# Kernel tuning notes

Hardware: AMD Instinct MI355X
Metric: run time of the kernel (lower is better)

## Reference

```python
import jax, jax.numpy as jnp
import numpy as np

N, C, S = 2, 512, 256
SCALE = 2.0

def setup_inputs() -> dict:
    key = jax.random.key(0)
    kq, kk, kv = jax.random.split(key, 3)
    q = jax.random.normal(kq, (N, C, S), dtype=jnp.float32)
    k = jax.random.normal(kk, (N, C, S), dtype=jnp.float32)
    v = jax.random.normal(kv, (N, C, S), dtype=jnp.float32)
    return {"q": q, "k": k, "v": v}

def reference(q, k, v):
    # q: (N,C,S) -> (N,C,1,S); k: (N,C,S) -> (N,1,C,S)
    # weights[n,c,d] = -sum_s |k[n,d,s] - q[n,c,s]| / scale
    diff = jnp.abs(k[:, None, :, :] - q[:, :, None, :])  # (N,C,C,S)
    weights = -(diff / SCALE).sum(axis=-1)               # (N,C,C)
    weights = jax.nn.softmax(weights, axis=-1)
    rep = jnp.einsum('ncd,nds->ncs', weights, v)         # (N,C,S)
    return rep
```

## Files before the change

### kernel.cpp

```cpp
#include <hip/hip_runtime.h>


constexpr int N_  = 2;
constexpr int C_  = 512;
constexpr int S_  = 256;
constexpr int TC  = 4;
constexpr int NT  = 512;
constexpr int NW  = NT / 64;
constexpr int SC  = 32;
constexpr int SCQ = SC / 4;
constexpr int NCH = S_ / SC;
constexpr int KF  = C_ * SCQ / NT;

template <int CTRL, int ROW_MASK>
__device__ __forceinline__ float dpp_add(float x) {
    int yi = __builtin_amdgcn_update_dpp(0, __float_as_int(x), CTRL, ROW_MASK, 0xf, true);
    return x + __int_as_float(yi);
}
template <int CTRL, int ROW_MASK>
__device__ __forceinline__ float dpp_max(float x) {
    int yi = __builtin_amdgcn_update_dpp(__float_as_int(x), __float_as_int(x), CTRL, ROW_MASK, 0xf, false);
    return fmaxf(x, __int_as_float(yi));
}
__device__ __forceinline__ float wave_sum_bcast(float x) {
    x = dpp_add<0x111, 0xf>(x);
    x = dpp_add<0x112, 0xf>(x);
    x = dpp_add<0x114, 0xf>(x);
    x = dpp_add<0x118, 0xf>(x);
    x = dpp_add<0x142, 0xa>(x);
    x = dpp_add<0x143, 0xc>(x);
    return __int_as_float(__builtin_amdgcn_readlane(__float_as_int(x), 63));
}
__device__ __forceinline__ float wave_max_bcast(float x) {
    x = dpp_max<0x111, 0xf>(x);
    x = dpp_max<0x112, 0xf>(x);
    x = dpp_max<0x114, 0xf>(x);
    x = dpp_max<0x118, 0xf>(x);
    x = dpp_max<0x142, 0xa>(x);
    x = dpp_max<0x143, 0xc>(x);
    return __int_as_float(__builtin_amdgcn_readlane(__float_as_int(x), 63));
}
__device__ __forceinline__ void fma4(float4& a, const float s, const float4& v) {
    a.x += s * v.x; a.y += s * v.y; a.z += s * v.z; a.w += s * v.w;
}

__global__ __launch_bounds__(NT, 1)
void laplace_attn_fused(const float* __restrict__ qg,
                        const float* __restrict__ kg,
                        const float* __restrict__ vg,
                        float* __restrict__ out) {
    __shared__ __align__(16) float ksm[2][C_][SC];
    __shared__ __align__(16) float qs[TC][S_];
    __shared__ __align__(16) float wt[C_][TC];
    __shared__ float4 red1[NW];
    __shared__ float4 red2[NW];
    float4 (*po)[TC][S_ / 4] = (float4 (*)[TC][S_ / 4])&ksm[0][0][0];

    const int b    = blockIdx.x;
    const int n    = b & 1;
    const int c0   = (b >> 1) * TC;
    const int tid  = threadIdx.x;
    const int w    = tid >> 6;
    const int lane = tid & 63;

    const float* kn = kg + (size_t)n * C_ * S_;
    const float* vn = vg + (size_t)n * C_ * S_;
    const float* qn = qg + ((size_t)n * C_ + c0) * S_;

    if (tid < TC * (S_ / 4)) {
        const int row = tid >> 6;
        const int col = (tid & 63) << 2;
        *(float4*)&qs[row][col] = *(const float4*)(qn + (size_t)row * S_ + col);
    }

    const int srow = tid >> 3;
    const int sqo  = tid & 7;
    const int sp   = (sqo + srow) & 7;

    float4 greg[KF];
    #pragma unroll
    for (int it = 0; it < KF; ++it) {
        const int row = srow + (it << 6);
        greg[it] = *(const float4*)(kn + (size_t)row * S_ + (sqo << 2));
    }
    #pragma unroll
    for (int it = 0; it < KF; ++it) {
        const int row = srow + (it << 6);
        *(float4*)&ksm[0][row][sp << 2] = greg[it];
    }
    __syncthreads();

    float dist0 = 0.f, dist1 = 0.f, dist2 = 0.f, dist3 = 0.f;
    int cur = 0;

    for (int ch = 0; ch < NCH; ++ch) {
        if (ch + 1 < NCH) {
            const float* kc = kn + (ch + 1) * SC;
            #pragma unroll
            for (int it = 0; it < KF; ++it) {
                const int row = srow + (it << 6);
                greg[it] = *(const float4*)(kc + (size_t)row * S_ + (sqo << 2));
            }
        }
        const int sb = ch * SC;
        #pragma unroll
        for (int j = 0; j < SCQ; ++j) {
            const int p = (j + tid) & 7;
            const float4 kf = *(const float4*)&ksm[cur][tid][p << 2];
            const int s = sb + (j << 2);
            const float4 qa = *(const float4*)&qs[0][s];
            const float4 qb = *(const float4*)&qs[1][s];
            const float4 qc = *(const float4*)&qs[2][s];
            const float4 qd = *(const float4*)&qs[3][s];
            dist0 += (fabsf(kf.x - qa.x) + fabsf(kf.y - qa.y))
                   + (fabsf(kf.z - qa.z) + fabsf(kf.w - qa.w));
            dist1 += (fabsf(kf.x - qb.x) + fabsf(kf.y - qb.y))
                   + (fabsf(kf.z - qb.z) + fabsf(kf.w - qb.w));
            dist2 += (fabsf(kf.x - qc.x) + fabsf(kf.y - qc.y))
                   + (fabsf(kf.z - qc.z) + fabsf(kf.w - qc.w));
            dist3 += (fabsf(kf.x - qd.x) + fabsf(kf.y - qd.y))
                   + (fabsf(kf.z - qd.z) + fabsf(kf.w - qd.w));
        }
        if (ch + 1 < NCH) {
            #pragma unroll
            for (int it = 0; it < KF; ++it) {
                const int row = srow + (it << 6);
                *(float4*)&ksm[cur ^ 1][row][sp << 2] = greg[it];
            }
            cur ^= 1;
        }
        __syncthreads();
    }

    float4 x;
    x.x = -0.5f * dist0; x.y = -0.5f * dist1;
    x.z = -0.5f * dist2; x.w = -0.5f * dist3;

    float4 mx;
    mx.x = wave_max_bcast(x.x); mx.y = wave_max_bcast(x.y);
    mx.z = wave_max_bcast(x.z); mx.w = wave_max_bcast(x.w);
    if (lane == 0) red1[w] = mx;
    __syncthreads();
    float4 M = red1[0];
    #pragma unroll
    for (int u = 1; u < NW; ++u) {
        const float4 r = red1[u];
        M.x = fmaxf(M.x, r.x); M.y = fmaxf(M.y, r.y);
        M.z = fmaxf(M.z, r.z); M.w = fmaxf(M.w, r.w);
    }

    float4 p;
    p.x = __expf(x.x - M.x); p.y = __expf(x.y - M.y);
    p.z = __expf(x.z - M.z); p.w = __expf(x.w - M.w);

    float4 sv;
    sv.x = wave_sum_bcast(p.x); sv.y = wave_sum_bcast(p.y);
    sv.z = wave_sum_bcast(p.z); sv.w = wave_sum_bcast(p.w);
    if (lane == 0) red2[w] = sv;
    __syncthreads();
    float4 L = red2[0];
    #pragma unroll
    for (int u = 1; u < NW; ++u) {
        const float4 r = red2[u];
        L.x += r.x; L.y += r.y; L.z += r.z; L.w += r.w;
    }
    p.x *= (1.f / L.x); p.y *= (1.f / L.y);
    p.z *= (1.f / L.z); p.w *= (1.f / L.w);
    *(float4*)&wt[tid][0] = p;
    __syncthreads();

    float4 o0 = make_float4(0.f, 0.f, 0.f, 0.f), o1 = o0, o2 = o0, o3 = o0;
    const int dbase = w << 6;
    #pragma unroll 8
    for (int dd = 0; dd < 64; ++dd) {
        const int d = dbase + dd;
        const float4 vv = *(const float4*)(vn + (size_t)d * S_ + (lane << 2));
        const float4 pw = *(const float4*)&wt[d][0];
        fma4(o0, pw.x, vv); fma4(o1, pw.y, vv);
        fma4(o2, pw.z, vv); fma4(o3, pw.w, vv);
    }
    po[w][0][lane] = o0; po[w][1][lane] = o1;
    po[w][2][lane] = o2; po[w][3][lane] = o3;
    __syncthreads();

    if (tid < TC * 64) {
        const int c    = tid >> 6;
        const int quad = tid & 63;
        float4 s = po[0][c][quad];
        #pragma unroll
        for (int u = 1; u < NW; ++u) {
            const float4 r = po[u][c][quad];
            s.x += r.x; s.y += r.y; s.z += r.z; s.w += r.w;
        }
        *(float4*)(out + ((size_t)n * C_ + c0 + c) * S_ + (quad << 2)) = s;
    }
}

extern "C" void kernel_launch(void* const* d_in, const int* in_sizes, int n_in,
                              void* d_out, int out_size, void* d_ws, size_t ws_size,
                              hipStream_t stream) {
    const float* q = (const float*)d_in[0];
    const float* k = (const float*)d_in[1];
    const float* v = (const float*)d_in[2];
    float* out = (float*)d_out;
    (void)d_ws; (void)ws_size;

    laplace_attn_fused<<<dim3(N_ * (C_ / TC)), dim3(NT), 0, stream>>>(q, k, v, out);
}
```

Baseline: 81.12 us.

## Double block size, split S across thread halves, read K directly from global

Blocks grow to 1024 threads. Each pair of threads splits the S dimension for one key row, and partial distances are combined through shared memory. The double-buffered LDS staging of K with its per-chunk barriers is removed: each thread streams its K row straight from global/L1 with float4 loads. The softmax runs only on the first 512 threads, and the V accumulation is spread over 16 waves. This aims for more parallelism per block and fewer syncs, at the cost of uncoalesced strided K loads (each thread reads a different row) and idle threads during the softmax.

Result: no change. 81.05 us (-0.1%).

```diff
diff --git a/kernel.cpp b/kernel.cpp
--- a/kernel.cpp
+++ b/kernel.cpp
@@ -5,12 +5,11 @@
 constexpr int C_  = 512;
 constexpr int S_  = 256;
 constexpr int TC  = 4;
-constexpr int NT  = 512;
-constexpr int NW  = NT / 64;
-constexpr int SC  = 32;
-constexpr int SCQ = SC / 4;
-constexpr int NCH = S_ / SC;
-constexpr int KF  = C_ * SCQ / NT;
+constexpr int NT  = 1024;
+constexpr int NWA = NT / 64;
+constexpr int NWH = C_ / 64;
+constexpr int SH  = S_ / 2;
+constexpr int DPW = C_ / NWA;
 
 template <int CTRL, int ROW_MASK>
 __device__ __forceinline__ float dpp_add(float x) {
@@ -44,17 +43,17 @@
     a.x += s * v.x; a.y += s * v.y; a.z += s * v.z; a.w += s * v.w;
 }
 
-__global__ __launch_bounds__(NT, 1)
+__global__ __launch_bounds__(NT, 4)
 void laplace_attn_fused(const float* __restrict__ qg,
                         const float* __restrict__ kg,
                         const float* __restrict__ vg,
                         float* __restrict__ out) {
-    __shared__ __align__(16) float ksm[2][C_][SC];
-    __shared__ __align__(16) float qs[TC][S_];
-    __shared__ __align__(16) float wt[C_][TC];
-    __shared__ float4 red1[NW];
-    __shared__ float4 red2[NW];
-    float4 (*po)[TC][S_ / 4] = (float4 (*)[TC][S_ / 4])&ksm[0][0][0];
+    __shared__ __align__(16) float  qs[TC][S_];
+    __shared__ __align__(16) float  dpart[2][C_][TC];
+    __shared__ __align__(16) float  wt[C_][TC];
+    __shared__ __align__(16) float4 po[NWA][TC][S_ / 4];
+    __shared__ float4 red1[NWH];
+    __shared__ float4 red2[NWH];
 
     const int b    = blockIdx.x;
     const int n    = b & 1;
@@ -62,6 +61,8 @@
     const int tid  = threadIdx.x;
     const int w    = tid >> 6;
     const int lane = tid & 63;
+    const int d    = tid & (C_ - 1);
+    const int h    = tid >> 9;
 
     const float* kn = kg + (size_t)n * C_ * S_;
     const float* vn = vg + (size_t)n * C_ * S_;
@@ -72,110 +73,83 @@
         const int col = (tid & 63) << 2;
         *(float4*)&qs[row][col] = *(const float4*)(qn + (size_t)row * S_ + col);
     }
+    __syncthreads();
 
-    const int srow = tid >> 3;
-    const int sqo  = tid & 7;
-    const int sp   = (sqo + srow) & 7;
+    const float4* kdv = (const float4*)(kn + (size_t)d * S_ + h * SH);
+    const int sb = h * SH;
+    float dist0 = 0.f, dist1 = 0.f, dist2 = 0.f, dist3 = 0.f;
 
-    float4 greg[KF];
-    #pragma unroll
-    for (int it = 0; it < KF; ++it) {
-        const int row = srow + (it << 6);
-        greg[it] = *(const float4*)(kn + (size_t)row * S_ + (sqo << 2));
+    #pragma unroll 8
+    for (int j = 0; j < SH / 4; ++j) {
+        const float4 kf = kdv[j];
+        const int s = sb + (j << 2);
+        const float4 qa = *(const float4*)&qs[0][s];
+        const float4 qb = *(const float4*)&qs[1][s];
+        const float4 qc = *(const float4*)&qs[2][s];
+        const float4 qd = *(const float4*)&qs[3][s];
+        dist0 += (fabsf(kf.x - qa.x) + fabsf(kf.y - qa.y))
+               + (fabsf(kf.z - qa.z) + fabsf(kf.w - qa.w));
+        dist1 += (fabsf(kf.x - qb.x) + fabsf(kf.y - qb.y))
+               + (fabsf(kf.z - qb.z) + fabsf(kf.w - qb.w));
+        dist2 += (fabsf(kf.x - qc.x) + fabsf(kf.y - qc.y))
+               + (fabsf(kf.z - qc.z) + fabsf(kf.w - qc.w));
+        dist3 += (fabsf(kf.x - qd.x) + fabsf(kf.y - qd.y))
+               + (fabsf(kf.z - qd.z) + fabsf(kf.w - qd.w));
     }
-    #pragma unroll
-    for (int it = 0; it < KF; ++it) {
-        const int row = srow + (it << 6);
-        *(float4*)&ksm[0][row][sp << 2] = greg[it];
+    *(float4*)&dpart[h][d][0] = make_float4(dist0, dist1, dist2, dist3);
+    __syncthreads();
+
+    const bool act = (tid < C_);
+    float4 p;
+    if (act) {
+        const float4 a0 = *(const float4*)&dpart[0][tid][0];
+        const float4 a1 = *(const float4*)&dpart[1][tid][0];
+        float4 x;
+        x.x = -0.5f * (a0.x + a1.x); x.y = -0.5f * (a0.y + a1.y);
+        x.z = -0.5f * (a0.z + a1.z); x.w = -0.5f * (a0.w + a1.w);
+        p = x;
+        float4 mx;
+        mx.x = wave_max_bcast(x.x); mx.y = wave_max_bcast(x.y);
+        mx.z = wave_max_bcast(x.z); mx.w = wave_max_bcast(x.w);
+        if (lane == 0) red1[w] = mx;
+    }
+    __syncthreads();
+    if (act) {
+        float4 M = red1[0];
+        #pragma unroll
+        for (int u = 1; u < NWH; ++u) {
+            const float4 r = red1[u];
+            M.x = fmaxf(M.x, r.x); M.y = fmaxf(M.y, r.y);
+            M.z = fmaxf(M.z, r.z); M.w = fmaxf(M.w, r.w);
+        }
+        p.x = __expf(p.x - M.x); p.y = __expf(p.y - M.y);
+        p.z = __expf(p.z - M.z); p.w = __expf(p.w - M.w);
+        float4 sv;
+        sv.x = wave_sum_bcast(p.x); sv.y = wave_sum_bcast(p.y);
+        sv.z = wave_sum_bcast(p.z); sv.w = wave_sum_bcast(p.w);
+        if (lane == 0) red2[w] = sv;
+    }
+    __syncthreads();
+    if (act) {
+        float4 L = red2[0];
+        #pragma unroll
+        for (int u = 1; u < NWH; ++u) {
+            const float4 r = red2[u];
+            L.x += r.x; L.y += r.y; L.z += r.z; L.w += r.w;
+        }
+        p.x *= (1.f / L.x); p.y *= (1.f / L.y);
+        p.z *= (1.f / L.z); p.w *= (1.f / L.w);
+        *(float4*)&wt[tid][0] = p;
     }
     __syncthreads();
 
-    float dist0 = 0.f, dist1 = 0.f, dist2 = 0.f, dist3 = 0.f;
-    int cur = 0;
-
-    for (int ch = 0; ch < NCH; ++ch) {
-        if (ch + 1 < NCH) {
-            const float* kc = kn + (ch + 1) * SC;
-            #pragma unroll
-            for (int it = 0; it < KF; ++it) {
-                const int row = srow + (it << 6);
-                greg[it] = *(const float4*)(kc + (size_t)row * S_ + (sqo << 2));
-            }
-        }
-        const int sb = ch * SC;
-        #pragma unroll
-        for (int j = 0; j < SCQ; ++j) {
-            const int p = (j + tid) & 7;
-            const float4 kf = *(const float4*)&ksm[cur][tid][p << 2];
-            const int s = sb + (j << 2);
-            const float4 qa = *(const float4*)&qs[0][s];
-            const float4 qb = *(const float4*)&qs[1][s];
-            const float4 qc = *(const float4*)&qs[2][s];
-            const float4 qd = *(const float4*)&qs[3][s];
-            dist0 += (fabsf(kf.x - qa.x) + fabsf(kf.y - qa.y))
-                   + (fabsf(kf.z - qa.z) + fabsf(kf.w - qa.w));
-            dist1 += (fabsf(kf.x - qb.x) + fabsf(kf.y - qb.y))
-                   + (fabsf(kf.z - qb.z) + fabsf(kf.w - qb.w));
-            dist2 += (fabsf(kf.x - qc.x) + fabsf(kf.y - qc.y))
-                   + (fabsf(kf.z - qc.z) + fabsf(kf.w - qc.w));
-            dist3 += (fabsf(kf.x - qd.x) + fabsf(kf.y - qd.y))
-                   + (fabsf(kf.z - qd.z) + fabsf(kf.w - qd.w));
-        }
-        if (ch + 1 < NCH) {
-            #pragma unroll
-            for (int it = 0; it < KF; ++it) {
-                const int row = srow + (it << 6);
-                *(float4*)&ksm[cur ^ 1][row][sp << 2] = greg[it];
-            }
-            cur ^= 1;
-        }
-        __syncthreads();
-    }
-
-    float4 x;
-    x.x = -0.5f * dist0; x.y = -0.5f * dist1;
-    x.z = -0.5f * dist2; x.w = -0.5f * dist3;
-
-    float4 mx;
-    mx.x = wave_max_bcast(x.x); mx.y = wave_max_bcast(x.y);
-    mx.z = wave_max_bcast(x.z); mx.w = wave_max_bcast(x.w);
-    if (lane == 0) red1[w] = mx;
-    __syncthreads();
-    float4 M = red1[0];
-    #pragma unroll
-    for (int u = 1; u < NW; ++u) {
-        const float4 r = red1[u];
-        M.x = fmaxf(M.x, r.x); M.y = fmaxf(M.y, r.y);
-        M.z = fmaxf(M.z, r.z); M.w = fmaxf(M.w, r.w);
-    }
-
-    float4 p;
-    p.x = __expf(x.x - M.x); p.y = __expf(x.y - M.y);
-    p.z = __expf(x.z - M.z); p.w = __expf(x.w - M.w);
-
-    float4 sv;
-    sv.x = wave_sum_bcast(p.x); sv.y = wave_sum_bcast(p.y);
-    sv.z = wave_sum_bcast(p.z); sv.w = wave_sum_bcast(p.w);
-    if (lane == 0) red2[w] = sv;
-    __syncthreads();
-    float4 L = red2[0];
-    #pragma unroll
-    for (int u = 1; u < NW; ++u) {
-        const float4 r = red2[u];
-        L.x += r.x; L.y += r.y; L.z += r.z; L.w += r.w;
-    }
-    p.x *= (1.f / L.x); p.y *= (1.f / L.y);
-    p.z *= (1.f / L.z); p.w *= (1.f / L.w);
-    *(float4*)&wt[tid][0] = p;
-    __syncthreads();
-
     float4 o0 = make_float4(0.f, 0.f, 0.f, 0.f), o1 = o0, o2 = o0, o3 = o0;
-    const int dbase = w << 6;
+    const int dbase = w * DPW;
     #pragma unroll 8
-    for (int dd = 0; dd < 64; ++dd) {
-        const int d = dbase + dd;
-        const float4 vv = *(const float4*)(vn + (size_t)d * S_ + (lane << 2));
-        const float4 pw = *(const float4*)&wt[d][0];
+    for (int dd = 0; dd < DPW; ++dd) {
+        const int dr = dbase + dd;
+        const float4 vv = *(const float4*)(vn + (size_t)dr * S_ + (lane << 2));
+        const float4 pw = *(const float4*)&wt[dr][0];
         fma4(o0, pw.x, vv); fma4(o1, pw.y, vv);
         fma4(o2, pw.z, vv); fma4(o3, pw.w, vv);
     }
@@ -188,7 +162,7 @@
         const int quad = tid & 63;
         float4 s = po[0][c][quad];
         #pragma unroll
-        for (int u = 1; u < NW; ++u) {
+        for (int u = 1; u < NWA; ++u) {
             const float4 r = po[u][c][quad];
             s.x += r.x; s.y += r.y; s.z += r.z; s.w += r.w;
         }
```
